# Kernel optimization log

Hardware: AMD Instinct MI355X
Metric: run time of the kernel (lower is better)

Reference implementation:

```python
import jax, jax.numpy as jnp
import numpy as np

FEATURE_DIM, HIDDEN_DIM, ATTN_DIM = 2048, 1024, 1024
B, L = 128, 196


def setup_inputs() -> dict:
    key = jax.random.key(0)
    ks = jax.random.split(key, 8)
    s_enc = 1.0 / np.sqrt(FEATURE_DIM)
    s_hid = 1.0 / np.sqrt(HIDDEN_DIM)
    s_full = 1.0 / np.sqrt(ATTN_DIM)
    return {
        "encoder_out": jax.random.normal(ks[0], (B, L, FEATURE_DIM), jnp.float32),
        "hidden": jax.random.normal(ks[1], (B, HIDDEN_DIM), jnp.float32),
        "W_enc": jax.random.uniform(ks[2], (FEATURE_DIM, ATTN_DIM), jnp.float32, -s_enc, s_enc),
        "b_enc": jax.random.uniform(ks[3], (ATTN_DIM,), jnp.float32, -s_enc, s_enc),
        "W_hid": jax.random.uniform(ks[4], (HIDDEN_DIM, ATTN_DIM), jnp.float32, -s_hid, s_hid),
        "b_hid": jax.random.uniform(ks[5], (ATTN_DIM,), jnp.float32, -s_hid, s_hid),
        "W_full": jax.random.uniform(ks[6], (ATTN_DIM,), jnp.float32, -s_full, s_full),
        "b_full": jax.random.uniform(ks[7], (1,), jnp.float32, -s_full, s_full),
    }


def reference(encoder_out, hidden, W_enc, b_enc, W_hid, b_hid, W_full, b_full):
    # attn1: (B, L, A)
    attn1 = jnp.einsum("blf,fa->bla", encoder_out, W_enc) + b_enc
    # attn2: (B, 1, A)
    attn2 = (hidden @ W_hid + b_hid)[:, None, :]
    attn = jax.nn.relu(attn1 + attn2)
    # scalar score per location: (B, L)
    scores = jnp.einsum("bla,a->bl", attn, W_full) + b_full[0]
    alpha = jax.nn.softmax(scores, axis=1)
    # weighted sum over L: (B, F)
    context = jnp.einsum("blf,bl->bf", encoder_out, alpha)
    return context, alpha
```

## Files before the change

### kernel.cpp

```cpp
#include <hip/hip_runtime.h>
#include <hip/hip_bf16.h>

typedef unsigned short u16;
typedef short s16x8 __attribute__((ext_vector_type(8)));
typedef unsigned int u32x2 __attribute__((ext_vector_type(2)));
typedef float f32x4 __attribute__((ext_vector_type(4)));

#define F_DIM 2048
#define A_DIM 1024
#define H_DIM 1024
#define BATCH 128
#define LLEN  196
#define MROWS (BATCH * LLEN)
#define MTILES (MROWS / 256)

__device__ __forceinline__ u16 f2b(float x) {
  union { float f; unsigned int u; } c; c.f = x;
  unsigned int r = (c.u + 0x7fffu + ((c.u >> 16) & 1u)) >> 16;
  return (u16)r;
}

__device__ __forceinline__ unsigned int f2b_pk(float a, float b) {
  unsigned int r;
  asm volatile("v_cvt_pk_bf16_f32 %0, %1, %2" : "=v"(r) : "v"(a), "v"(b));
  return r;
}

__device__ __forceinline__ void gload_lds16(const void* g, void* l) {
  __builtin_amdgcn_global_load_lds((const __attribute__((address_space(1))) void*)g,
                                   (__attribute__((address_space(3))) void*)l, 16, 0, 0);
}

__global__ __launch_bounds__(256) void prep_kernel(
    const float* __restrict__ W, u16* __restrict__ WT,
    const float* __restrict__ hidden, const float* __restrict__ W_hid,
    const float* __restrict__ b_hid, const float* __restrict__ b_enc,
    float* __restrict__ attn2p) {
  int t = threadIdx.x;
  if (blockIdx.x < 2048) {
    __shared__ float tile[32][33];
    int id = blockIdx.x;
    int kb = (id & 63) * 32, ab = (id >> 6) * 32;
    int r = t >> 3, c = (t & 7) * 4;
    float4 v = *(const float4*)&W[(size_t)(kb + r) * A_DIM + ab + c];
    tile[r][c] = v.x; tile[r][c + 1] = v.y; tile[r][c + 2] = v.z; tile[r][c + 3] = v.w;
    __syncthreads();
    ushort4 o;
    o.x = f2b(tile[c + 0][r]);
    o.y = f2b(tile[c + 1][r]);
    o.z = f2b(tile[c + 2][r]);
    o.w = f2b(tile[c + 3][r]);
    *(ushort4*)&WT[(size_t)(ab + r) * F_DIM + kb + c] = o;
  } else {
    __shared__ float hl[8][128];
    int id = blockIdx.x - 2048;
    int a  = (id & 3) * 256 + t;
    int b0 = ((id >> 2) & 15) * 8;
    int k0 = (id >> 6) * 128;
    {
      int j = t >> 5, kk = (t & 31) * 4;
      float4 v = *(const float4*)&hidden[(size_t)(b0 + j) * H_DIM + k0 + kk];
      hl[j][kk + 0] = v.x; hl[j][kk + 1] = v.y; hl[j][kk + 2] = v.z; hl[j][kk + 3] = v.w;
    }
    __syncthreads();
    float acc[8] = {0.f, 0.f, 0.f, 0.f, 0.f, 0.f, 0.f, 0.f};
    #pragma unroll 4
    for (int k = 0; k < 128; ++k) {
      float w = W_hid[(size_t)(k0 + k) * A_DIM + a];
      #pragma unroll
      for (int j = 0; j < 8; ++j) acc[j] = fmaf(hl[j][k], w, acc[j]);
    }
    if ((id >> 6) == 0) {
      float bias = b_hid[a] + b_enc[a];
      #pragma unroll
      for (int j = 0; j < 8; ++j) acc[j] += bias;
    }
    #pragma unroll
    for (int j = 0; j < 8; ++j) atomicAdd(&attn2p[(size_t)(b0 + j) * A_DIM + a], acc[j]);
  }
}

__global__ __launch_bounds__(512, 2) void gemm_score(
    const float* __restrict__ enc, const u16* __restrict__ WT,
    const float* __restrict__ attn2p, const float* __restrict__ W_full,
    float* __restrict__ scores) {
  __shared__ __align__(16) u16 As[2 * 16384];
  __shared__ __align__(16) u16 Bs[2 * 16384];

  int i = blockIdx.x;
  int g = i >> 5, r = i & 31;
  int y = r >> 3, gi = r & 7;
  int mt = g * 8 + gi;
  if (mt >= MTILES) return;
  int m0 = mt * 256, n0 = y * 256;
  int t = threadIdx.x;
  int lane = t & 63, wave = t >> 6;
  int wr = wave >> 2, wc = wave & 3;
  int c16 = lane & 15, quad = lane >> 4;

  const float* aP = enc + (size_t)(m0 + (t >> 2)) * F_DIM + (t & 3) * 4;
  int awo[4];
  #pragma unroll
  for (int s = 0; s < 4; ++s)
    awo[s] = (t >> 2) * 64 + ((t & 3) & 1) * 4
           + (((s * 2 + ((t & 3) >> 1)) ^ ((t >> 2) & 7)) * 8);
  const u16* bgp = WT + (size_t)(n0 + (t >> 3)) * F_DIM + ((t & 7) ^ ((t >> 3) & 7)) * 8;

  const int akey = c16 & 7;
  int gsw[2];
  gsw[0] = ((0 * 4 + quad) ^ akey) * 8;
  gsw[1] = ((1 * 4 + quad) ^ akey) * 8;
  const int aro = (wr * 128 + c16) * 64;
  const int bro = (wc * 64 + c16) * 64;

  f32x4 acc[8][4];
  #pragma unroll
  for (int mi = 0; mi < 8; ++mi)
    #pragma unroll
    for (int ni = 0; ni < 4; ++ni) acc[mi][ni] = (f32x4){0.f, 0.f, 0.f, 0.f};

  s16x8 af[4][2], bf[2][2];
  float4 R0lo[4], R0hi[4], R1lo[4], R1hi[4];

#define ALD(RX, half, kt_) do {                                                 \
    const float* p_ = aP + (size_t)(half) * 128 * F_DIM + (kt_) * 64;           \
    RX[0] = *(const float4*)(p_);                                               \
    RX[1] = *(const float4*)(p_ + 16);                                          \
    RX[2] = *(const float4*)(p_ + 32);                                          \
    RX[3] = *(const float4*)(p_ + 48);                                          \
  } while (0)

#define AWR(RX, cb, half) do {                                                  \
    _Pragma("unroll")                                                           \
    for (int s_ = 0; s_ < 4; ++s_) {                                            \
      u32x2 w_; w_.x = f2b_pk(RX[s_].x, RX[s_].y);                              \
      w_.y = f2b_pk(RX[s_].z, RX[s_].w);                                        \
      *(u32x2*)&As[(cb) * 16384 + (half) * 8192 + awo[s_]] = w_;                \
    }                                                                           \
  } while (0)

#define BGL(cb, kt_) do {                                                       \
    _Pragma("unroll")                                                           \
    for (int s_ = 0; s_ < 4; ++s_)                                              \
      gload_lds16(bgp + (size_t)s_ * 64 * F_DIM + (size_t)(kt_) * 64,           \
                  Bs + (cb) * 16384 + s_ * 4096 + wave * 512);                  \
  } while (0)

#define DSRA(cb, mh)                                                            \
    _Pragma("unroll")                                                           \
    for (int i_ = 0; i_ < 4; ++i_)                                              \
      _Pragma("unroll")                                                         \
      for (int h_ = 0; h_ < 2; ++h_)                                            \
        af[i_][h_] = *(const s16x8*)&As[(cb) * 16384 + aro                      \
                                        + ((mh) * 4 + i_) * 1024 + gsw[h_]];

#define DSRB(cb, nh)                                                            \
    _Pragma("unroll")                                                           \
    for (int j_ = 0; j_ < 2; ++j_)                                              \
      _Pragma("unroll")                                                         \
      for (int h_ = 0; h_ < 2; ++h_)                                            \
        bf[j_][h_] = *(const s16x8*)&Bs[(cb) * 16384 + bro                      \
                                        + ((nh) * 2 + j_) * 1024 + gsw[h_]];

#define PHTAIL(mh, nh) do {                                                     \
    __builtin_amdgcn_s_barrier();                                               \
    asm volatile("s_waitcnt lgkmcnt(0)" ::: "memory");                          \
    __builtin_amdgcn_s_setprio(1);                                              \
    _Pragma("unroll")                                                           \
    for (int i_ = 0; i_ < 4; ++i_)                                              \
      _Pragma("unroll")                                                         \
      for (int j_ = 0; j_ < 2; ++j_)                                            \
        _Pragma("unroll")                                                       \
        for (int h_ = 0; h_ < 2; ++h_)                                          \
          acc[(mh) * 4 + i_][(nh) * 2 + j_] =                                   \
              __builtin_amdgcn_mfma_f32_16x16x32_bf16(                          \
                  af[i_][h_], bf[j_][h_],                                       \
                  acc[(mh) * 4 + i_][(nh) * 2 + j_], 0, 0, 0);                  \
    __builtin_amdgcn_s_setprio(0);                                              \
    __builtin_amdgcn_s_barrier();                                               \
  } while (0)

#define GROUP(T_, RB_, WB_, WLO_, WHI_, LLO_, LHI_) do {                        \
    int kB_ = min((T_) + 1, 31);                                                \
    int kA_ = min((T_) + 2, 31);                                                \
                                                                        \
    DSRA(RB_, 0); DSRB(RB_, 0);                                                 \
    BGL(WB_, kB_);                                                              \
    ALD(LLO_, 0, kA_);                                                          \
    PHTAIL(0, 0);                                                               \
                                                                        \
    DSRB(RB_, 1);                                                               \
    ALD(LHI_, 1, kA_);                                                          \
    AWR(WLO_, WB_, 0);                                                          \
    PHTAIL(0, 1);                                                               \
                                                                        \
    DSRA(RB_, 1); DSRB(RB_, 0);                                                 \
    AWR(WHI_, WB_, 1);                                                          \
    PHTAIL(1, 0);                                                               \
                                                                        \
    DSRB(RB_, 1);                                                               \
    asm volatile("s_waitcnt vmcnt(8)" ::: "memory");                            \
    PHTAIL(1, 1);                                                               \
  } while (0)

  ALD(R0lo, 0, 0);
  ALD(R0hi, 1, 0);
  BGL(0, 0);
  asm volatile("s_waitcnt vmcnt(4)" ::: "memory");
  AWR(R0lo, 0, 0);
  AWR(R0hi, 0, 1);
  ALD(R1lo, 0, 1);
  ALD(R1hi, 1, 1);
  asm volatile("s_waitcnt vmcnt(8) lgkmcnt(0)" ::: "memory");
  __builtin_amdgcn_s_barrier();

  #pragma unroll 1
  for (int T = 0; T < 32; T += 2) {
    GROUP(T,     0, 1, R1lo, R1hi, R0lo, R0hi);
    GROUP(T + 1, 1, 0, R0lo, R0hi, R1lo, R1hi);
  }
#undef GROUP
#undef PHTAIL
#undef DSRA
#undef DSRB
#undef BGL
#undef AWR
#undef ALD

  int bfirst = m0 / LLEN;
  int bnd1 = (bfirst + 1) * LLEN, bnd2 = (bfirst + 2) * LLEN;
  int b1c = min(bfirst + 1, BATCH - 1), b2c = min(bfirst + 2, BATCH - 1);
  float wf[4], a2v0[4], a2v1[4], a2v2[4];
  #pragma unroll
  for (int ni = 0; ni < 4; ++ni) {
    int col = n0 + wc * 64 + ni * 16 + c16;
    wf[ni]   = W_full[col];
    a2v0[ni] = attn2p[(size_t)bfirst * A_DIM + col];
    a2v1[ni] = attn2p[(size_t)b1c * A_DIM + col];
    a2v2[ni] = attn2p[(size_t)b2c * A_DIM + col];
  }
  #pragma unroll
  for (int mi = 0; mi < 8; ++mi) {
    #pragma unroll
    for (int rr = 0; rr < 4; ++rr) {
      int row_g = m0 + wr * 128 + mi * 16 + quad * 4 + rr;
      float p = 0.f;
      #pragma unroll
      for (int ni = 0; ni < 4; ++ni) {
        float a2 = row_g >= bnd1 ? (row_g >= bnd2 ? a2v2[ni] : a2v1[ni]) : a2v0[ni];
        float v = acc[mi][ni][rr] + a2;
        v = fmaxf(v, 0.f);
        p = fmaf(v, wf[ni], p);
      }
      p += __shfl_xor(p, 1);
      p += __shfl_xor(p, 2);
      p += __shfl_xor(p, 4);
      p += __shfl_xor(p, 8);
      if (c16 == 0) atomicAdd(&scores[row_g], p);
    }
  }
}

__global__ __launch_bounds__(256) void context_kernel(
    const float* __restrict__ enc, const float* __restrict__ scores,
    float* __restrict__ alpha_out, float* __restrict__ out) {
  __shared__ float al[LLEN];
  __shared__ float red[8];
  __shared__ float4 part[4][64];
  int b = blockIdx.y, t = threadIdx.x;
  float s = (t < LLEN) ? scores[b * LLEN + t] : -3.0e38f;
  float m = s;
  #pragma unroll
  for (int o = 1; o <= 32; o <<= 1) m = fmaxf(m, __shfl_xor(m, o));
  if ((t & 63) == 0) red[t >> 6] = m;
  __syncthreads();
  m = fmaxf(fmaxf(red[0], red[1]), fmaxf(red[2], red[3]));
  float e = (t < LLEN) ? expf(s - m) : 0.f;
  float sum = e;
  #pragma unroll
  for (int o = 1; o <= 32; o <<= 1) sum += __shfl_xor(sum, o);
  if ((t & 63) == 0) red[4 + (t >> 6)] = sum;
  __syncthreads();
  sum = red[4] + red[5] + red[6] + red[7];
  float av = e / sum;
  if (t < LLEN) {
    al[t] = av;
    if (blockIdx.x == 0) alpha_out[b * LLEN + t] = av;
  }
  __syncthreads();
  int f4 = blockIdx.x * 64 + (t & 63);
  int lq = t >> 6;
  const float4* e4 = (const float4*)enc
                   + ((size_t)b * LLEN + lq * 49) * (F_DIM / 4) + f4;
  float4 acc = {0.f, 0.f, 0.f, 0.f};
  #pragma unroll 7
  for (int j = 0; j < 49; ++j) {
    float4 v = e4[(size_t)j * (F_DIM / 4)];
    float a = al[lq * 49 + j];
    acc.x = fmaf(v.x, a, acc.x);
    acc.y = fmaf(v.y, a, acc.y);
    acc.z = fmaf(v.z, a, acc.z);
    acc.w = fmaf(v.w, a, acc.w);
  }
  part[lq][t & 63] = acc;
  __syncthreads();
  if (t < 64) {
    float4 p0 = part[0][t], p1 = part[1][t], p2 = part[2][t], p3 = part[3][t];
    float4 sv;
    sv.x = (p0.x + p1.x) + (p2.x + p3.x);
    sv.y = (p0.y + p1.y) + (p2.y + p3.y);
    sv.z = (p0.z + p1.z) + (p2.z + p3.z);
    sv.w = (p0.w + p1.w) + (p2.w + p3.w);
    *(float4*)(out + (size_t)b * F_DIM + (size_t)(blockIdx.x * 64 + t) * 4) = sv;
  }
}

extern "C" void kernel_launch(void* const* d_in, const int* in_sizes, int n_in,
                              void* d_out, int out_size, void* d_ws, size_t ws_size,
                              hipStream_t stream) {
  const float* enc    = (const float*)d_in[0];
  const float* hidden = (const float*)d_in[1];
  const float* W_enc  = (const float*)d_in[2];
  const float* b_enc  = (const float*)d_in[3];
  const float* W_hid  = (const float*)d_in[4];
  const float* b_hid  = (const float*)d_in[5];
  const float* W_full = (const float*)d_in[6];
  float* out = (float*)d_out;
  float* alpha_out = out + (size_t)BATCH * F_DIM;

  const size_t wt_bytes = (size_t)A_DIM * F_DIM * sizeof(u16);
  const size_t a2_bytes = (size_t)BATCH * A_DIM * sizeof(float);
  const size_t sc_bytes = (size_t)MROWS * sizeof(float);
  char* ws = (char*)d_ws;
  u16*   WT     = (u16*)ws;
  float* attn2p = (float*)(ws + wt_bytes);
  float* scores = (float*)(ws + wt_bytes + a2_bytes);

  hipMemsetAsync(attn2p, 0, a2_bytes + sc_bytes, stream);

  prep_kernel<<<dim3(2048 + 512), 256, 0, stream>>>(W_enc, WT, hidden, W_hid, b_hid, b_enc, attn2p);
  gemm_score<<<dim3(416), 512, 0, stream>>>(enc, WT, attn2p, W_full, scores);
  context_kernel<<<dim3(8, BATCH), 256, 0, stream>>>(enc, scores, alpha_out, out);
}
```

Before: 503.6 us.

## Pre-convert encoder activations to bf16 and load GEMM A tiles directly to LDS

When the workspace is large enough, a new prep-kernel branch converts the whole encoder_out to bf16 in a separate pass. The GEMM then streams A tiles with global_load_lds like B, which removes the register staging and in-loop fp32-to-bf16 conversion and simplifies the pipeline to single-stage prefetch. The cost is an extra full read of the fp32 encoder plus a write and re-read of a ~100MB bf16 copy. A fallback path keeps a reordered version of the old kernel. Whether the big path runs depends on the workspace size the harness provides.

```diff
diff --git a/kernel.cpp b/kernel.cpp
--- a/kernel.cpp
+++ b/kernel.cpp
@@ -4,6 +4,7 @@
 typedef unsigned short u16;
 typedef short s16x8 __attribute__((ext_vector_type(8)));
 typedef unsigned int u32x2 __attribute__((ext_vector_type(2)));
+typedef unsigned int u32x4 __attribute__((ext_vector_type(4)));
 typedef float f32x4 __attribute__((ext_vector_type(4)));
 
 #define F_DIM 2048
@@ -35,7 +36,8 @@
     const float* __restrict__ W, u16* __restrict__ WT,
     const float* __restrict__ hidden, const float* __restrict__ W_hid,
     const float* __restrict__ b_hid, const float* __restrict__ b_enc,
-    float* __restrict__ attn2p) {
+    float* __restrict__ attn2p,
+    const float* __restrict__ enc, u16* __restrict__ encB) {
   int t = threadIdx.x;
   if (blockIdx.x < 2048) {
     __shared__ float tile[32][33];
@@ -51,7 +53,7 @@
     o.z = f2b(tile[c + 2][r]);
     o.w = f2b(tile[c + 3][r]);
     *(ushort4*)&WT[(size_t)(ab + r) * F_DIM + kb + c] = o;
-  } else {
+  } else if (blockIdx.x < 2560) {
     __shared__ float hl[8][128];
     int id = blockIdx.x - 2048;
     int a  = (id & 3) * 256 + t;
@@ -77,11 +79,19 @@
     }
     #pragma unroll
     for (int j = 0; j < 8; ++j) atomicAdd(&attn2p[(size_t)(b0 + j) * A_DIM + a], acc[j]);
-  }
-}
-
-__global__ __launch_bounds__(512, 2) void gemm_score(
-    const float* __restrict__ enc, const u16* __restrict__ WT,
+  } else {
+    int r = blockIdx.x - 2560;
+    const float4* sp = (const float4*)(enc + (size_t)r * F_DIM) + t * 2;
+    float4 a = sp[0], b = sp[1];
+    u32x4 w;
+    w.x = f2b_pk(a.x, a.y); w.y = f2b_pk(a.z, a.w);
+    w.z = f2b_pk(b.x, b.y); w.w = f2b_pk(b.z, b.w);
+    *(u32x4*)(encB + (size_t)r * F_DIM + t * 8) = w;
+  }
+}
+
+__global__ __launch_bounds__(512, 2) void gemm_score_a(
+    const u16* __restrict__ encB, const u16* __restrict__ WT,
     const float* __restrict__ attn2p, const float* __restrict__ W_full,
     float* __restrict__ scores) {
   __shared__ __align__(16) u16 As[2 * 16384];
@@ -98,13 +108,8 @@
   int wr = wave >> 2, wc = wave & 3;
   int c16 = lane & 15, quad = lane >> 4;
 
-  const float* aP = enc + (size_t)(m0 + (t >> 2)) * F_DIM + (t & 3) * 4;
-  int awo[4];
-  #pragma unroll
-  for (int s = 0; s < 4; ++s)
-    awo[s] = (t >> 2) * 64 + ((t & 3) & 1) * 4
-           + (((s * 2 + ((t & 3) >> 1)) ^ ((t >> 2) & 7)) * 8);
-  const u16* bgp = WT + (size_t)(n0 + (t >> 3)) * F_DIM + ((t & 7) ^ ((t >> 3) & 7)) * 8;
+  const u16* agp = encB + (size_t)(m0 + (t >> 3)) * F_DIM + ((t & 7) ^ ((t >> 3) & 7)) * 8;
+  const u16* bgp = WT   + (size_t)(n0 + (t >> 3)) * F_DIM + ((t & 7) ^ ((t >> 3) & 7)) * 8;
 
   const int akey = c16 & 7;
   int gsw[2];
@@ -119,24 +124,13 @@
     #pragma unroll
     for (int ni = 0; ni < 4; ++ni) acc[mi][ni] = (f32x4){0.f, 0.f, 0.f, 0.f};
 
-  s16x8 af[4][2], bf[2][2];
-  float4 R0lo[4], R0hi[4], R1lo[4], R1hi[4];
-
-#define ALD(RX, half, kt_) do {                                                 \
-    const float* p_ = aP + (size_t)(half) * 128 * F_DIM + (kt_) * 64;           \
-    RX[0] = *(const float4*)(p_);                                               \
-    RX[1] = *(const float4*)(p_ + 16);                                          \
-    RX[2] = *(const float4*)(p_ + 32);                                          \
-    RX[3] = *(const float4*)(p_ + 48);                                          \
-  } while (0)
-
-#define AWR(RX, cb, half) do {                                                  \
-    _Pragma("unroll")                                                           \
-    for (int s_ = 0; s_ < 4; ++s_) {                                            \
-      u32x2 w_; w_.x = f2b_pk(RX[s_].x, RX[s_].y);                              \
-      w_.y = f2b_pk(RX[s_].z, RX[s_].w);                                        \
-      *(u32x2*)&As[(cb) * 16384 + (half) * 8192 + awo[s_]] = w_;                \
-    }                                                                           \
+  s16x8 af[4][2], bf0[2][2], bf1[2][2];
+
+#define AGL(cb, kt_) do {                                                       \
+    _Pragma("unroll")                                                           \
+    for (int s_ = 0; s_ < 4; ++s_)                                              \
+      gload_lds16(agp + (size_t)s_ * 64 * F_DIM + (size_t)(kt_) * 64,           \
+                  As + (cb) * 16384 + s_ * 4096 + wave * 512);                  \
   } while (0)
 
 #define BGL(cb, kt_) do {                                                       \
@@ -154,15 +148,15 @@
         af[i_][h_] = *(const s16x8*)&As[(cb) * 16384 + aro                      \
                                         + ((mh) * 4 + i_) * 1024 + gsw[h_]];
 
-#define DSRB(cb, nh)                                                            \
+#define DSRB(BF, cb, nh)                                                        \
     _Pragma("unroll")                                                           \
     for (int j_ = 0; j_ < 2; ++j_)                                              \
       _Pragma("unroll")                                                         \
       for (int h_ = 0; h_ < 2; ++h_)                                            \
-        bf[j_][h_] = *(const s16x8*)&Bs[(cb) * 16384 + bro                      \
+        BF[j_][h_] = *(const s16x8*)&Bs[(cb) * 16384 + bro                      \
                                         + ((nh) * 2 + j_) * 1024 + gsw[h_]];
 
-#define PHTAIL(mh, nh) do {                                                     \
+#define PHTAIL(BF, mh, nh) do {                                                 \
     __builtin_amdgcn_s_barrier();                                               \
     asm volatile("s_waitcnt lgkmcnt(0)" ::: "memory");                          \
     __builtin_amdgcn_s_setprio(1);                                              \
@@ -174,58 +168,36 @@
         for (int h_ = 0; h_ < 2; ++h_)                                          \
           acc[(mh) * 4 + i_][(nh) * 2 + j_] =                                   \
               __builtin_amdgcn_mfma_f32_16x16x32_bf16(                          \
-                  af[i_][h_], bf[j_][h_],                                       \
+                  af[i_][h_], BF[j_][h_],                                       \
                   acc[(mh) * 4 + i_][(nh) * 2 + j_], 0, 0, 0);                  \
     __builtin_amdgcn_s_setprio(0);                                              \
     __builtin_amdgcn_s_barrier();                                               \
   } while (0)
 
-#define GROUP(T_, RB_, WB_, WLO_, WHI_, LLO_, LHI_) do {                        \
-    int kB_ = min((T_) + 1, 31);                                                \
-    int kA_ = min((T_) + 2, 31);                                                \
-                                                                        \
-    DSRA(RB_, 0); DSRB(RB_, 0);                                                 \
-    BGL(WB_, kB_);                                                              \
-    ALD(LLO_, 0, kA_);                                                          \
-    PHTAIL(0, 0);                                                               \
-                                                                        \
-    DSRB(RB_, 1);                                                               \
-    ALD(LHI_, 1, kA_);                                                          \
-    AWR(WLO_, WB_, 0);                                                          \
-    PHTAIL(0, 1);                                                               \
-                                                                        \
-    DSRA(RB_, 1); DSRB(RB_, 0);                                                 \
-    AWR(WHI_, WB_, 1);                                                          \
-    PHTAIL(1, 0);                                                               \
-                                                                        \
-    DSRB(RB_, 1);                                                               \
-    asm volatile("s_waitcnt vmcnt(8)" ::: "memory");                            \
-    PHTAIL(1, 1);                                                               \
-  } while (0)
-
-  ALD(R0lo, 0, 0);
-  ALD(R0hi, 1, 0);
+#define GROUPA(T_, RB_, WB_) do {                                               \
+    int kS_ = min((T_) + 1, 31);                                                \
+     DSRA(RB_, 0); DSRB(bf0, RB_, 0); AGL(WB_, kS_); PHTAIL(bf0, 0, 0);\
+     DSRB(bf1, RB_, 1); BGL(WB_, kS_);              PHTAIL(bf1, 0, 1); \
+     DSRA(RB_, 1);                                   PHTAIL(bf0, 1, 0);\
+     asm volatile("s_waitcnt vmcnt(0)" ::: "memory"); PHTAIL(bf1, 1, 1);\
+  } while (0)
+
+  AGL(0, 0);
   BGL(0, 0);
-  asm volatile("s_waitcnt vmcnt(4)" ::: "memory");
-  AWR(R0lo, 0, 0);
-  AWR(R0hi, 0, 1);
-  ALD(R1lo, 0, 1);
-  ALD(R1hi, 1, 1);
-  asm volatile("s_waitcnt vmcnt(8) lgkmcnt(0)" ::: "memory");
+  asm volatile("s_waitcnt vmcnt(0) lgkmcnt(0)" ::: "memory");
   __builtin_amdgcn_s_barrier();
 
   #pragma unroll 1
   for (int T = 0; T < 32; T += 2) {
-    GROUP(T,     0, 1, R1lo, R1hi, R0lo, R0hi);
-    GROUP(T + 1, 1, 0, R0lo, R0hi, R1lo, R1hi);
-  }
-#undef GROUP
+    GROUPA(T,     0, 1);
+    GROUPA(T + 1, 1, 0);
+  }
+#undef GROUPA
 #undef PHTAIL
 #undef DSRA
 #undef DSRB
 #undef BGL
-#undef AWR
-#undef ALD
+#undef AGL
 
   int bfirst = m0 / LLEN;
   int bnd1 = (bfirst + 1) * LLEN, bnd2 = (bfirst + 2) * LLEN;
@@ -261,6 +233,178 @@
   }
 }
 
+__global__ __launch_bounds__(512, 2) void gemm_score_b(
+    const float* __restrict__ enc, const u16* __restrict__ WT,
+    const float* __restrict__ attn2p, const float* __restrict__ W_full,
+    float* __restrict__ scores) {
+  __shared__ __align__(16) u16 As[2 * 16384];
+  __shared__ __align__(16) u16 Bs[2 * 16384];
+
+  int i = blockIdx.x;
+  int g = i >> 5, r = i & 31;
+  int y = r >> 3, gi = r & 7;
+  int mt = g * 8 + gi;
+  if (mt >= MTILES) return;
+  int m0 = mt * 256, n0 = y * 256;
+  int t = threadIdx.x;
+  int lane = t & 63, wave = t >> 6;
+  int wr = wave >> 2, wc = wave & 3;
+  int c16 = lane & 15, quad = lane >> 4;
+
+  const float* aP = enc + (size_t)(m0 + (t >> 2)) * F_DIM + (t & 3) * 4;
+  int awo[4];
+  #pragma unroll
+  for (int s = 0; s < 4; ++s)
+    awo[s] = (t >> 2) * 64 + ((t & 3) & 1) * 4
+           + (((s * 2 + ((t & 3) >> 1)) ^ ((t >> 2) & 7)) * 8);
+  const u16* bgp = WT + (size_t)(n0 + (t >> 3)) * F_DIM + ((t & 7) ^ ((t >> 3) & 7)) * 8;
+
+  const int akey = c16 & 7;
+  int gsw[2];
+  gsw[0] = ((0 * 4 + quad) ^ akey) * 8;
+  gsw[1] = ((1 * 4 + quad) ^ akey) * 8;
+  const int aro = (wr * 128 + c16) * 64;
+  const int bro = (wc * 64 + c16) * 64;
+
+  f32x4 acc[8][4];
+  #pragma unroll
+  for (int mi = 0; mi < 8; ++mi)
+    #pragma unroll
+    for (int ni = 0; ni < 4; ++ni) acc[mi][ni] = (f32x4){0.f, 0.f, 0.f, 0.f};
+
+  s16x8 af[4][2], bf[2][2];
+  float4 R0lo[4], R0hi[4], R1lo[4], R1hi[4];
+
+#define ALD(RX, half, kt_) do {                                                 \
+    const float* p_ = aP + (size_t)(half) * 128 * F_DIM + (kt_) * 64;           \
+    RX[0] = *(const float4*)(p_);                                               \
+    RX[1] = *(const float4*)(p_ + 16);                                          \
+    RX[2] = *(const float4*)(p_ + 32);                                          \
+    RX[3] = *(const float4*)(p_ + 48);                                          \
+  } while (0)
+
+#define AWR(RX, cb, half) do {                                                  \
+    _Pragma("unroll")                                                           \
+    for (int s_ = 0; s_ < 4; ++s_) {                                            \
+      u32x2 w_; w_.x = f2b_pk(RX[s_].x, RX[s_].y);                              \
+      w_.y = f2b_pk(RX[s_].z, RX[s_].w);                                        \
+      *(u32x2*)&As[(cb) * 16384 + (half) * 8192 + awo[s_]] = w_;                \
+    }                                                                           \
+  } while (0)
+
+#define BGL(cb, kt_) do {                                                       \
+    _Pragma("unroll")                                                           \
+    for (int s_ = 0; s_ < 4; ++s_)                                              \
+      gload_lds16(bgp + (size_t)s_ * 64 * F_DIM + (size_t)(kt_) * 64,           \
+                  Bs + (cb) * 16384 + s_ * 4096 + wave * 512);                  \
+  } while (0)
+
+#define DSRA(cb, mh)                                                            \
+    _Pragma("unroll")                                                           \
+    for (int i_ = 0; i_ < 4; ++i_)                                              \
+      _Pragma("unroll")                                                         \
+      for (int h_ = 0; h_ < 2; ++h_)                                            \
+        af[i_][h_] = *(const s16x8*)&As[(cb) * 16384 + aro                      \
+                                        + ((mh) * 4 + i_) * 1024 + gsw[h_]];
+
+#define DSRB(cb, nh)                                                            \
+    _Pragma("unroll")                                                           \
+    for (int j_ = 0; j_ < 2; ++j_)                                              \
+      _Pragma("unroll")                                                         \
+      for (int h_ = 0; h_ < 2; ++h_)                                            \
+        bf[j_][h_] = *(const s16x8*)&Bs[(cb) * 16384 + bro                      \
+                                        + ((nh) * 2 + j_) * 1024 + gsw[h_]];
+
+#define PHTAIL(mh, nh) do {                                                     \
+    __builtin_amdgcn_s_barrier();                                               \
+    asm volatile("s_waitcnt lgkmcnt(0)" ::: "memory");                          \
+    __builtin_amdgcn_s_setprio(1);                                              \
+    _Pragma("unroll")                                                           \
+    for (int i_ = 0; i_ < 4; ++i_)                                              \
+      _Pragma("unroll")                                                         \
+      for (int j_ = 0; j_ < 2; ++j_)                                            \
+        _Pragma("unroll")                                                       \
+        for (int h_ = 0; h_ < 2; ++h_)                                          \
+          acc[(mh) * 4 + i_][(nh) * 2 + j_] =                                   \
+              __builtin_amdgcn_mfma_f32_16x16x32_bf16(                          \
+                  af[i_][h_], bf[j_][h_],                                       \
+                  acc[(mh) * 4 + i_][(nh) * 2 + j_], 0, 0, 0);                  \
+    __builtin_amdgcn_s_setprio(0);                                               \
+    __builtin_amdgcn_s_barrier();                                               \
+  } while (0)
+
+#define GROUP(T_, RB_, WB_, WLO_, WHI_, LLO_, LHI_) do {                        \
+    int kB_ = min((T_) + 1, 31);                                                \
+    int kA_ = min((T_) + 2, 31);                                                \
+     DSRA(RB_, 0); DSRB(RB_, 0); AWR(WLO_, WB_, 0); BGL(WB_, kB_);      \
+    PHTAIL(0, 0);                                                               \
+     DSRB(RB_, 1); AWR(WHI_, WB_, 1); ALD(LLO_, 0, kA_);                \
+    PHTAIL(0, 1);                                                               \
+     DSRA(RB_, 1); DSRB(RB_, 0); ALD(LHI_, 1, kA_);                     \
+    PHTAIL(1, 0);                                                               \
+     DSRB(RB_, 1);                                                      \
+    asm volatile("s_waitcnt vmcnt(8)" ::: "memory");                            \
+    PHTAIL(1, 1);                                                               \
+  } while (0)
+
+  ALD(R0lo, 0, 0);
+  ALD(R0hi, 1, 0);
+  BGL(0, 0);
+  asm volatile("s_waitcnt vmcnt(4)" ::: "memory");
+  AWR(R0lo, 0, 0);
+  AWR(R0hi, 0, 1);
+  ALD(R1lo, 0, 1);
+  ALD(R1hi, 1, 1);
+  asm volatile("s_waitcnt vmcnt(8) lgkmcnt(0)" ::: "memory");
+  __builtin_amdgcn_s_barrier();
+
+  #pragma unroll 1
+  for (int T = 0; T < 32; T += 2) {
+    GROUP(T,     0, 1, R1lo, R1hi, R0lo, R0hi);
+    GROUP(T + 1, 1, 0, R0lo, R0hi, R1lo, R1hi);
+  }
+#undef GROUP
+#undef PHTAIL
+#undef DSRA
+#undef DSRB
+#undef BGL
+#undef AWR
+#undef ALD
+
+  int bfirst = m0 / LLEN;
+  int bnd1 = (bfirst + 1) * LLEN, bnd2 = (bfirst + 2) * LLEN;
+  int b1c = min(bfirst + 1, BATCH - 1), b2c = min(bfirst + 2, BATCH - 1);
+  float wf[4], a2v0[4], a2v1[4], a2v2[4];
+  #pragma unroll
+  for (int ni = 0; ni < 4; ++ni) {
+    int col = n0 + wc * 64 + ni * 16 + c16;
+    wf[ni]   = W_full[col];
+    a2v0[ni] = attn2p[(size_t)bfirst * A_DIM + col];
+    a2v1[ni] = attn2p[(size_t)b1c * A_DIM + col];
+    a2v2[ni] = attn2p[(size_t)b2c * A_DIM + col];
+  }
+  #pragma unroll
+  for (int mi = 0; mi < 8; ++mi) {
+    #pragma unroll
+    for (int rr = 0; rr < 4; ++rr) {
+      int row_g = m0 + wr * 128 + mi * 16 + quad * 4 + rr;
+      float p = 0.f;
+      #pragma unroll
+      for (int ni = 0; ni < 4; ++ni) {
+        float a2 = row_g >= bnd1 ? (row_g >= bnd2 ? a2v2[ni] : a2v1[ni]) : a2v0[ni];
+        float v = acc[mi][ni][rr] + a2;
+        v = fmaxf(v, 0.f);
+        p = fmaf(v, wf[ni], p);
+      }
+      p += __shfl_xor(p, 1);
+      p += __shfl_xor(p, 2);
+      p += __shfl_xor(p, 4);
+      p += __shfl_xor(p, 8);
+      if (c16 == 0) atomicAdd(&scores[row_g], p);
+    }
+  }
+}
+
 __global__ __launch_bounds__(256) void context_kernel(
     const float* __restrict__ enc, const float* __restrict__ scores,
     float* __restrict__ alpha_out, float* __restrict__ out) {
@@ -328,17 +472,28 @@
   float* out = (float*)d_out;
   float* alpha_out = out + (size_t)BATCH * F_DIM;
 
-  const size_t wt_bytes = (size_t)A_DIM * F_DIM * sizeof(u16);
-  const size_t a2_bytes = (size_t)BATCH * A_DIM * sizeof(float);
-  const size_t sc_bytes = (size_t)MROWS * sizeof(float);
+  const size_t wt_bytes   = (size_t)A_DIM * F_DIM * sizeof(u16);
+  const size_t a2_bytes   = (size_t)BATCH * A_DIM * sizeof(float);
+  const size_t sc_bytes   = (size_t)MROWS * sizeof(float);
+  const size_t encb_bytes = (size_t)MROWS * F_DIM * sizeof(u16);
   char* ws = (char*)d_ws;
   u16*   WT     = (u16*)ws;
   float* attn2p = (float*)(ws + wt_bytes);
   float* scores = (float*)(ws + wt_bytes + a2_bytes);
+  u16*   encB   = (u16*)(ws + wt_bytes + a2_bytes + sc_bytes);
+
+  const bool bigws = ws_size >= wt_bytes + a2_bytes + sc_bytes + encb_bytes;
 
   hipMemsetAsync(attn2p, 0, a2_bytes + sc_bytes, stream);
 
-  prep_kernel<<<dim3(2048 + 512), 256, 0, stream>>>(W_enc, WT, hidden, W_hid, b_hid, b_enc, attn2p);
-  gemm_score<<<dim3(416), 512, 0, stream>>>(enc, WT, attn2p, W_full, scores);
+  if (bigws) {
+    prep_kernel<<<dim3(2048 + 512 + MROWS), 256, 0, stream>>>(
+        W_enc, WT, hidden, W_hid, b_hid, b_enc, attn2p, enc, encB);
+    gemm_score_a<<<dim3(416), 512, 0, stream>>>(encB, WT, attn2p, W_full, scores);
+  } else {
+    prep_kernel<<<dim3(2048 + 512), 256, 0, stream>>>(
+        W_enc, WT, hidden, W_hid, b_hid, b_enc, attn2p, enc, encB);
+    gemm_score_b<<<dim3(416), 512, 0, stream>>>(enc, WT, attn2p, W_full, scores);
+  }
   context_kernel<<<dim3(8, BATCH), 256, 0, stream>>>(enc, scores, alpha_out, out);
 }
```

After: 470.9 us. 1.07x faster.
